# Optimization experiments

Hardware: AMD Instinct MI355X
Metric: run time of the kernel (lower is better)

The kernel has to match this reference:

```python
import jax, jax.numpy as jnp
import numpy as np

B, L, D = 8, 8192, 768  # trees, leaves per tree, d_in == d_hidden


def setup_inputs() -> dict:
    key = jax.random.key(0)
    ks = jax.random.split(key, 5)
    scale = 0.02  # keep gates out of saturation
    return {
        "leaf_emb": jax.random.normal(ks[0], (B, L, D), dtype=jnp.float32),
        "W_iou": jax.random.normal(ks[1], (3 * D, D), dtype=jnp.float32) * scale,
        "b_iou": jnp.zeros((3 * D,), dtype=jnp.float32),
        "U_iou": jax.random.normal(ks[2], (3 * D, D), dtype=jnp.float32) * scale,
        "W_f": jax.random.normal(ks[3], (D, D), dtype=jnp.float32) * scale,
        "b_f": jnp.zeros((D,), dtype=jnp.float32),
        "U_f": jax.random.normal(ks[4], (D, D), dtype=jnp.float32) * scale,
    }


def reference(leaf_emb, W_iou, b_iou, U_iou, W_f, b_f, U_f):
    """Child-Sum Tree-LSTM over a perfect binary tree, level-synchronous.

    Leaves: h = embedding, c = 0 (matches the torch module's leaf case).
    Internal node with children (l, r):
      h_sum = h_l + h_r; x = h_sum / 2
      i,o,u = split(W_iou x + b_iou + U_iou h_sum)
      f_k   = sigmoid(W_f x + b_f + U_f h_k)   per child
      c = sigmoid(i)*tanh(u) + f_l*c_l + f_r*c_r;  h = sigmoid(o)*tanh(c)
    Returns stacked (h_root, c_root): [2, B, D].
    """
    h = leaf_emb                      # [B, n, D]
    c = jnp.zeros_like(h)
    while h.shape[1] > 1:             # static trace-time loop over depth (13 levels)
        hl, hr = h[:, 0::2], h[:, 1::2]   # [B, n/2, D]
        cl, cr = c[:, 0::2], c[:, 1::2]
        h_sum = hl + hr
        x = h_sum * 0.5               # x_j = h_sum / num_children (==2)
        iou = jnp.einsum('bnd,gd->bng', x, W_iou) + b_iou \
            + jnp.einsum('bnd,gd->bng', h_sum, U_iou)
        i, o, u = jnp.split(iou, 3, axis=-1)
        wfx = jnp.einsum('bnd,hd->bnh', x, W_f) + b_f
        f_l = jax.nn.sigmoid(wfx + jnp.einsum('bnd,hd->bnh', hl, U_f))
        f_r = jax.nn.sigmoid(wfx + jnp.einsum('bnd,hd->bnh', hr, U_f))
        c = jax.nn.sigmoid(i) * jnp.tanh(u) + f_l * cl + f_r * cr
        h = jax.nn.sigmoid(o) * jnp.tanh(c)
    return jnp.stack([h[:, 0], c[:, 0]])  # [2, B, D]
```

## Files before the change

kernel.cpp:

```cpp
#include <hip/hip_runtime.h>


typedef _Float16 half8 __attribute__((ext_vector_type(8)));
typedef float f32x4 __attribute__((ext_vector_type(4)));

#define ROWB 1536
#define NT 24
#define BUFB 36864
#define MATB 1179648

__device__ __forceinline__ float sigm(float x){ return 1.f/(1.f+__expf(-x)); }
__device__ __forceinline__ float tanhfast(float x){ return 1.f - 2.f/(1.f+__expf(2.f*x)); }

__device__ __forceinline__ void gload16(const void* g, void* l){
  __builtin_amdgcn_global_load_lds((const __attribute__((address_space(1))) void*)g,
                                   (__attribute__((address_space(3))) void*)l, 16, 0, 0);
}

__global__ void prep_weights(const float* __restrict__ Wiou, const float* __restrict__ Uiou,
                             const float* __restrict__ Wf, const float* __restrict__ Uf,
                             _Float16* __restrict__ Bw)
{
    const int n1 = 2304 * 768, n2 = n1 + 589824, n3 = n2 + 589824;
    int stride = gridDim.x * blockDim.x;
    for (int idx = blockIdx.x * blockDim.x + threadIdx.x; idx < n3; idx += stride) {
        float v;
        if (idx < n1)      v = __fmaf_rn(0.5f, Wiou[idx], Uiou[idx]);
        else if (idx < n2) { int k = idx - n1; v = __fmaf_rn(0.5f, Wf[k], Uf[k]); }
        else               { int k = idx - n2; v = 0.5f * Wf[k]; }
        Bw[idx] = (_Float16)v;
    }
}

__global__ void cast_leaves(const float* __restrict__ x, _Float16* __restrict__ h, int n8)
{
    int stride = gridDim.x * blockDim.x;
    for (int i = blockIdx.x * blockDim.x + threadIdx.x; i < n8; i += stride) {
        float4 v0 = ((const float4*)x)[2 * i];
        float4 v1 = ((const float4*)x)[2 * i + 1];
        half8 o = { (_Float16)v0.x, (_Float16)v0.y, (_Float16)v0.z, (_Float16)v0.w,
                    (_Float16)v1.x, (_Float16)v1.y, (_Float16)v1.z, (_Float16)v1.w };
        ((half8*)h)[i] = o;
    }
}

__global__ __launch_bounds__(256, 2) void tree_level(
    const _Float16* __restrict__ Hc, const float* __restrict__ Cc,
    const _Float16* __restrict__ Bw,
    const float* __restrict__ biou, const float* __restrict__ bfv,
    _Float16* __restrict__ Hn, float* __restrict__ Cn,
    float* __restrict__ outH, float* __restrict__ outC,
    int M, int mblocks, int firstLevel, int finalLevel)
{
    __shared__ __align__(16) char smem[2 * BUFB];
    const int tid = threadIdx.x;
    const int lane = tid & 63;
    const int w = tid >> 6;
    const int wm = w >> 1;
    const int wd = w & 1;

    const int nwg = mblocks * 12;
    const int orig = blockIdx.x;
    const int xcd = orig & 7, qx = nwg >> 3, rx = nwg & 7;
    const int v = (xcd < rx ? xcd * (qx + 1) : rx * (qx + 1) + (xcd - rx) * qx) + (orig >> 3);
    const int d0c = v / mblocks;
    const int mb = v - d0c * mblocks;
    const int mBase = mb * 128;
    const int d0 = d0c * 64;

    const int l3 = lane >> 3, j = lane & 7;
    const int rbase = w * 8 + l3;
    const int jjA = j ^ l3;
    unsigned offH[4];
#pragma unroll
    for (int s = 0; s < 4; ++s) {
        int gr = mBase + s * 32 + rbase;
        if (gr >= M) gr = M - 1;
        offH[s] = (unsigned)(2 * gr + (jjA >> 2)) * ROWB + (jjA & 3) * 16;
    }
    const int pB = w * 8 + l3;
    const int jjB = j ^ (pB & 7);
    const unsigned offWcol = (unsigned)(d0 + 2 * pB + (jjB >> 2)) * ROWB + (jjB & 3) * 16;
    const int wK = w * 1024;

#define STAGE(bi, ko) do { \
    _Pragma("unroll") for (int s = 0; s < 4; ++s) \
        gload16((const char*)Hc + offH[s] + (ko), smem + (bi) * BUFB + s * 4096 + wK); \
    _Pragma("unroll") for (int s = 0; s < 5; ++s) \
        gload16((const char*)Bw + (size_t)s * MATB + offWcol + (ko), \
                smem + (bi) * BUFB + 16384 + s * 4096 + wK); \
} while (0)

    const int q = lane >> 4;
    const int lr = lane & 15;
    int offA[4], offB[2];
#pragma unroll
    for (int fm = 0; fm < 4; ++fm) {
        int r = wm * 64 + fm * 16 + lr;
        offA[fm] = r * 128 + ((q ^ (r & 7)) * 16);
    }
#pragma unroll
    for (int fd = 0; fd < 2; ++fd) {
        int cl = wd * 32 + fd * 16 + lr;
        int p = cl >> 1;
        int jb = ((cl & 1) * 4 + q) ^ (p & 7);
        offB[fd] = 16384 + p * 128 + jb * 16;
    }

    f32x4 acc[5][4][2];
#pragma unroll
    for (int g = 0; g < 5; ++g)
#pragma unroll
        for (int a = 0; a < 4; ++a)
#pragma unroll
            for (int b = 0; b < 2; ++b)
                acc[g][a][b] = (f32x4){0.f, 0.f, 0.f, 0.f};

    STAGE(0, 0);
    int cur = 0;
    for (int kt = 0; kt < NT; ++kt) {
        if (kt + 1 < NT) {
            STAGE(cur ^ 1, (kt + 1) * 64);
            asm volatile("s_waitcnt vmcnt(9)" ::: "memory");
        } else {
            asm volatile("s_waitcnt vmcnt(0)" ::: "memory");
        }
        __builtin_amdgcn_s_barrier();
        __builtin_amdgcn_sched_barrier(0);
        const char* bb = smem + cur * BUFB;
        half8 hl[4], hr[4];
#pragma unroll
        for (int fm = 0; fm < 4; ++fm) {
            hl[fm] = *(const half8*)(bb + offA[fm]);
            hr[fm] = *(const half8*)(bb + (offA[fm] ^ 64));
        }
        __builtin_amdgcn_s_setprio(1);
#pragma unroll
        for (int fd = 0; fd < 2; ++fd) {
            const char* bp = bb + offB[fd];
            half8 b0 = *(const half8*)(bp);
            half8 b1 = *(const half8*)(bp + 4096);
            half8 b2 = *(const half8*)(bp + 8192);
            half8 b3 = *(const half8*)(bp + 12288);
            half8 b4 = *(const half8*)(bp + 16384);
#pragma unroll
            for (int fm = 0; fm < 4; ++fm) {
                half8 hs = hl[fm] + hr[fm];
                acc[0][fm][fd] = __builtin_amdgcn_mfma_f32_16x16x32_f16(hs, b0, acc[0][fm][fd], 0, 0, 0);
                acc[1][fm][fd] = __builtin_amdgcn_mfma_f32_16x16x32_f16(hs, b1, acc[1][fm][fd], 0, 0, 0);
                acc[2][fm][fd] = __builtin_amdgcn_mfma_f32_16x16x32_f16(hs, b2, acc[2][fm][fd], 0, 0, 0);
                acc[3][fm][fd] = __builtin_amdgcn_mfma_f32_16x16x32_f16(hl[fm], b3, acc[3][fm][fd], 0, 0, 0);
                acc[3][fm][fd] = __builtin_amdgcn_mfma_f32_16x16x32_f16(hr[fm], b4, acc[3][fm][fd], 0, 0, 0);
                acc[4][fm][fd] = __builtin_amdgcn_mfma_f32_16x16x32_f16(hl[fm], b4, acc[4][fm][fd], 0, 0, 0);
                acc[4][fm][fd] = __builtin_amdgcn_mfma_f32_16x16x32_f16(hr[fm], b3, acc[4][fm][fd], 0, 0, 0);
            }
        }
        __builtin_amdgcn_s_setprio(0);
        if (kt + 1 < NT) __builtin_amdgcn_s_barrier();
        cur ^= 1;
    }

#pragma unroll
    for (int fd = 0; fd < 2; ++fd) {
        const int col = d0 + wd * 32 + fd * 16 + lr;
        const float bi = biou[col];
        const float bo = biou[768 + col];
        const float bu = biou[1536 + col];
        const float bf = bfv[col];
#pragma unroll
        for (int fm = 0; fm < 4; ++fm) {
            const int rb = mBase + wm * 64 + fm * 16 + q * 4;
#pragma unroll
            for (int r4 = 0; r4 < 4; ++r4) {
                int row = rb + r4;
                if (row < M) {
                    float iv = acc[0][fm][fd][r4] + bi;
                    float ov = acc[1][fm][fd][r4] + bo;
                    float uv = acc[2][fm][fd][r4] + bu;
                    float fl = sigm(acc[3][fm][fd][r4] + bf);
                    float fr = sigm(acc[4][fm][fd][r4] + bf);
                    float clv = 0.f, crv = 0.f;
                    if (!firstLevel) {
                        clv = Cc[(size_t)(2 * row) * 768 + col];
                        crv = Cc[(size_t)(2 * row + 1) * 768 + col];
                    }
                    float c = sigm(iv) * tanhfast(uv) + fl * clv + fr * crv;
                    float h = sigm(ov) * tanhfast(c);
                    if (finalLevel) {
                        outH[row * 768 + col] = h;
                        outC[row * 768 + col] = c;
                    } else {
                        Hn[(size_t)row * 768 + col] = (_Float16)h;
                        Cn[(size_t)row * 768 + col] = c;
                    }
                }
            }
        }
    }
}

extern "C" void kernel_launch(void* const* d_in, const int* in_sizes, int n_in,
                              void* d_out, int out_size, void* d_ws, size_t ws_size,
                              hipStream_t stream)
{
    const float* leaf = (const float*)d_in[0];
    const float* Wiou = (const float*)d_in[1];
    const float* biou = (const float*)d_in[2];
    const float* Uiou = (const float*)d_in[3];
    const float* Wf   = (const float*)d_in[4];
    const float* bfv  = (const float*)d_in[5];
    const float* Uf   = (const float*)d_in[6];

    char* ws = (char*)d_ws;
    _Float16* Bw = (_Float16*)(ws);
    _Float16* H0 = (_Float16*)(ws + 5898240);
    _Float16* H1 = (_Float16*)(ws + 106561536);
    float*    C0 = (float*)(ws + 156893184);
    float*    C1 = (float*)(ws + 257556480);

    prep_weights<<<1024, 256, 0, stream>>>(Wiou, Uiou, Wf, Uf, Bw);
    cast_leaves<<<2048, 256, 0, stream>>>(leaf, H0, 50331648 / 8);

    float* out = (float*)d_out;
    _Float16* Hc = H0; _Float16* Hn = H1;
    float* Cc = C1; float* Cn = C0;
    int rows = 65536, level = 0;
    while (rows > 8) {
        int M = rows >> 1;
        int fin = (M == 8) ? 1 : 0;
        int mblocks = (M + 127) / 128;
        tree_level<<<mblocks * 12, 256, 0, stream>>>(Hc, Cc, Bw, biou, bfv,
            Hn, Cn, fin ? out : (float*)nullptr, fin ? out + 6144 : (float*)nullptr,
            M, mblocks, level == 0 ? 1 : 0, fin);
        _Float16* th = Hc; Hc = Hn; Hn = th;
        float* tc = Cc; Cc = Cn; Cn = tc;
        rows = M; ++level;
    }
}
```

Measured before the change: 1.064 ms.

## Issue next-tile prefetch after LDS fragment reads and reorder block-to-tile mapping

The loop now reads all A and B fragments from LDS into registers, issues the global-to-LDS prefetch for the next K tile, and only then runs the MFMA chain. The wait becomes vmcnt(0) at the top of each iteration. The block index decomposition changes so that neighbouring workgroups share an M block across the 12 column chunks, which should improve reuse of the H rows in L2. The s_setprio hints are removed. This adds register pressure from holding 10 B fragments plus hs, and the full vmcnt(0) wait may expose load latency if the MFMA work does not cover it.

```diff
diff --git a/kernel.cpp b/kernel.cpp
--- a/kernel.cpp
+++ b/kernel.cpp
@@ -63,8 +63,8 @@
     const int orig = blockIdx.x;
     const int xcd = orig & 7, qx = nwg >> 3, rx = nwg & 7;
     const int v = (xcd < rx ? xcd * (qx + 1) : rx * (qx + 1) + (xcd - rx) * qx) + (orig >> 3);
-    const int d0c = v / mblocks;
-    const int mb = v - d0c * mblocks;
+    const int mb = v / 12;
+    const int d0c = v - mb * 12;
     const int mBase = mb * 128;
     const int d0 = d0c * 64;
 
@@ -119,43 +119,40 @@
     STAGE(0, 0);
     int cur = 0;
     for (int kt = 0; kt < NT; ++kt) {
-        if (kt + 1 < NT) {
-            STAGE(cur ^ 1, (kt + 1) * 64);
-            asm volatile("s_waitcnt vmcnt(9)" ::: "memory");
-        } else {
-            asm volatile("s_waitcnt vmcnt(0)" ::: "memory");
-        }
+        asm volatile("s_waitcnt vmcnt(0)" ::: "memory");
         __builtin_amdgcn_s_barrier();
-        __builtin_amdgcn_sched_barrier(0);
         const char* bb = smem + cur * BUFB;
-        half8 hl[4], hr[4];
+        half8 hl[4], hr[4], hs[4];
+        half8 bfrag[2][5];
 #pragma unroll
         for (int fm = 0; fm < 4; ++fm) {
             hl[fm] = *(const half8*)(bb + offA[fm]);
             hr[fm] = *(const half8*)(bb + (offA[fm] ^ 64));
         }
-        __builtin_amdgcn_s_setprio(1);
 #pragma unroll
         for (int fd = 0; fd < 2; ++fd) {
             const char* bp = bb + offB[fd];
-            half8 b0 = *(const half8*)(bp);
-            half8 b1 = *(const half8*)(bp + 4096);
-            half8 b2 = *(const half8*)(bp + 8192);
-            half8 b3 = *(const half8*)(bp + 12288);
-            half8 b4 = *(const half8*)(bp + 16384);
+#pragma unroll
+            for (int t = 0; t < 5; ++t)
+                bfrag[fd][t] = *(const half8*)(bp + t * 4096);
+        }
+        if (kt + 1 < NT) STAGE(cur ^ 1, (kt + 1) * 64);
+        __builtin_amdgcn_sched_barrier(0);
+#pragma unroll
+        for (int fm = 0; fm < 4; ++fm) hs[fm] = hl[fm] + hr[fm];
+#pragma unroll
+        for (int fd = 0; fd < 2; ++fd) {
 #pragma unroll
             for (int fm = 0; fm < 4; ++fm) {
-                half8 hs = hl[fm] + hr[fm];
-                acc[0][fm][fd] = __builtin_amdgcn_mfma_f32_16x16x32_f16(hs, b0, acc[0][fm][fd], 0, 0, 0);
-                acc[1][fm][fd] = __builtin_amdgcn_mfma_f32_16x16x32_f16(hs, b1, acc[1][fm][fd], 0, 0, 0);
-                acc[2][fm][fd] = __builtin_amdgcn_mfma_f32_16x16x32_f16(hs, b2, acc[2][fm][fd], 0, 0, 0);
-                acc[3][fm][fd] = __builtin_amdgcn_mfma_f32_16x16x32_f16(hl[fm], b3, acc[3][fm][fd], 0, 0, 0);
-                acc[3][fm][fd] = __builtin_amdgcn_mfma_f32_16x16x32_f16(hr[fm], b4, acc[3][fm][fd], 0, 0, 0);
-                acc[4][fm][fd] = __builtin_amdgcn_mfma_f32_16x16x32_f16(hl[fm], b4, acc[4][fm][fd], 0, 0, 0);
-                acc[4][fm][fd] = __builtin_amdgcn_mfma_f32_16x16x32_f16(hr[fm], b3, acc[4][fm][fd], 0, 0, 0);
+                acc[0][fm][fd] = __builtin_amdgcn_mfma_f32_16x16x32_f16(hs[fm], bfrag[fd][0], acc[0][fm][fd], 0, 0, 0);
+                acc[1][fm][fd] = __builtin_amdgcn_mfma_f32_16x16x32_f16(hs[fm], bfrag[fd][1], acc[1][fm][fd], 0, 0, 0);
+                acc[2][fm][fd] = __builtin_amdgcn_mfma_f32_16x16x32_f16(hs[fm], bfrag[fd][2], acc[2][fm][fd], 0, 0, 0);
+                acc[3][fm][fd] = __builtin_amdgcn_mfma_f32_16x16x32_f16(hl[fm], bfrag[fd][3], acc[3][fm][fd], 0, 0, 0);
+                acc[3][fm][fd] = __builtin_amdgcn_mfma_f32_16x16x32_f16(hr[fm], bfrag[fd][4], acc[3][fm][fd], 0, 0, 0);
+                acc[4][fm][fd] = __builtin_amdgcn_mfma_f32_16x16x32_f16(hl[fm], bfrag[fd][4], acc[4][fm][fd], 0, 0, 0);
+                acc[4][fm][fd] = __builtin_amdgcn_mfma_f32_16x16x32_f16(hr[fm], bfrag[fd][3], acc[4][fm][fd], 0, 0, 0);
             }
         }
-        __builtin_amdgcn_s_setprio(0);
         if (kt + 1 < NT) __builtin_amdgcn_s_barrier();
         cur ^= 1;
     }
```

After: 1.229 ms. 1.16x slower.

## Halve output-column tile to 32 and raise occupancy to three workgroups per CU

Applied to the files above, without the earlier changes.

Shrinks each workgroup's output tile from 64 to 32 hidden columns, doubling the grid and halving accumulator registers and weight shared-memory staging. This lets launch bounds target three resident workgroups per CU. It also changes the order of grid blocks, so that blocks sharing the same M rows land next to each other. It also re-maps the weight loads so fewer global-to-LDS copies are issued per stage, and loads hl/hr inside the MFMA loop. The cost is that each H tile is now read by twice as many workgroups and each A fragment is reused over fewer MFMAs.

```diff
diff --git a/kernel.cpp b/kernel.cpp
--- a/kernel.cpp
+++ b/kernel.cpp
@@ -6,8 +6,8 @@
 
 #define ROWB 1536
 #define NT 24
-#define BUFB 36864
-#define MATB 1179648
+#define BUFB 26624
+#define BOFF 16384
 
 __device__ __forceinline__ float sigm(float x){ return 1.f/(1.f+__expf(-x)); }
 __device__ __forceinline__ float tanhfast(float x){ return 1.f - 2.f/(1.f+__expf(2.f*x)); }
@@ -44,7 +44,7 @@
     }
 }
 
-__global__ __launch_bounds__(256, 2) void tree_level(
+__global__ __launch_bounds__(256, 3) void tree_level(
     const _Float16* __restrict__ Hc, const float* __restrict__ Cc,
     const _Float16* __restrict__ Bw,
     const float* __restrict__ biou, const float* __restrict__ bfv,
@@ -59,140 +59,134 @@
     const int wm = w >> 1;
     const int wd = w & 1;
 
-    const int nwg = mblocks * 12;
+    const int nwg = mblocks * 24;
     const int orig = blockIdx.x;
     const int xcd = orig & 7, qx = nwg >> 3, rx = nwg & 7;
     const int v = (xcd < rx ? xcd * (qx + 1) : rx * (qx + 1) + (xcd - rx) * qx) + (orig >> 3);
-    const int d0c = v / mblocks;
-    const int mb = v - d0c * mblocks;
+    const int mb = v / 24;
+    const int d0c = v - mb * 24;
     const int mBase = mb * 128;
-    const int d0 = d0c * 64;
+    const int d0 = d0c * 32;
 
     const int l3 = lane >> 3, j = lane & 7;
-    const int rbase = w * 8 + l3;
-    const int jjA = j ^ l3;
-    unsigned offH[4];
+    const int jj0 = j ^ l3;
+    unsigned offHa[4], offWb[3];
+    int dstA[4], dstB[3];
 #pragma unroll
     for (int s = 0; s < 4; ++s) {
-        int gr = mBase + s * 32 + rbase;
+        int u = s * 4 + w;
+        int gr = mBase + u * 8 + l3;
         if (gr >= M) gr = M - 1;
-        offH[s] = (unsigned)(2 * gr + (jjA >> 2)) * ROWB + (jjA & 3) * 16;
-    }
-    const int pB = w * 8 + l3;
-    const int jjB = j ^ (pB & 7);
-    const unsigned offWcol = (unsigned)(d0 + 2 * pB + (jjB >> 2)) * ROWB + (jjB & 3) * 16;
-    const int wK = w * 1024;
+        offHa[s] = (unsigned)(2 * gr + (jj0 >> 2)) * ROWB + (jj0 & 3) * 16;
+        dstA[s] = u * 1024;
+    }
+#pragma unroll
+    for (int s = 0; s < 3; ++s) {
+        int i = s * 4 + w;
+        if (i >= 10) i -= 2;
+        int t = i >> 1, half = i & 1;
+        int p = half * 8 + l3;
+        int cl = 2 * p + (jj0 >> 2);
+        offWb[s] = (unsigned)(t * 768 + d0 + cl) * ROWB + (jj0 & 3) * 16;
+        dstB[s] = BOFF + t * 2048 + half * 1024;
+    }
 
 #define STAGE(bi, ko) do { \
     _Pragma("unroll") for (int s = 0; s < 4; ++s) \
-        gload16((const char*)Hc + offH[s] + (ko), smem + (bi) * BUFB + s * 4096 + wK); \
-    _Pragma("unroll") for (int s = 0; s < 5; ++s) \
-        gload16((const char*)Bw + (size_t)s * MATB + offWcol + (ko), \
-                smem + (bi) * BUFB + 16384 + s * 4096 + wK); \
+        gload16((const char*)Hc + offHa[s] + (ko), smem + (bi) * BUFB + dstA[s]); \
+    _Pragma("unroll") for (int s = 0; s < 3; ++s) \
+        gload16((const char*)Bw + offWb[s] + (ko), smem + (bi) * BUFB + dstB[s]); \
 } while (0)
 
     const int q = lane >> 4;
     const int lr = lane & 15;
-    int offA[4], offB[2];
+    int offA[4];
 #pragma unroll
     for (int fm = 0; fm < 4; ++fm) {
         int r = wm * 64 + fm * 16 + lr;
         offA[fm] = r * 128 + ((q ^ (r & 7)) * 16);
     }
-#pragma unroll
-    for (int fd = 0; fd < 2; ++fd) {
-        int cl = wd * 32 + fd * 16 + lr;
+    int offB;
+    {
+        int cl = wd * 16 + lr;
         int p = cl >> 1;
         int jb = ((cl & 1) * 4 + q) ^ (p & 7);
-        offB[fd] = 16384 + p * 128 + jb * 16;
-    }
-
-    f32x4 acc[5][4][2];
+        offB = BOFF + p * 128 + jb * 16;
+    }
+
+    f32x4 acc[5][4];
 #pragma unroll
     for (int g = 0; g < 5; ++g)
 #pragma unroll
         for (int a = 0; a < 4; ++a)
-#pragma unroll
-            for (int b = 0; b < 2; ++b)
-                acc[g][a][b] = (f32x4){0.f, 0.f, 0.f, 0.f};
+            acc[g][a] = (f32x4){0.f, 0.f, 0.f, 0.f};
 
     STAGE(0, 0);
     int cur = 0;
     for (int kt = 0; kt < NT; ++kt) {
         if (kt + 1 < NT) {
             STAGE(cur ^ 1, (kt + 1) * 64);
-            asm volatile("s_waitcnt vmcnt(9)" ::: "memory");
+            asm volatile("s_waitcnt vmcnt(7)" ::: "memory");
         } else {
             asm volatile("s_waitcnt vmcnt(0)" ::: "memory");
         }
         __builtin_amdgcn_s_barrier();
         __builtin_amdgcn_sched_barrier(0);
         const char* bb = smem + cur * BUFB;
-        half8 hl[4], hr[4];
+        half8 b0 = *(const half8*)(bb + offB);
+        half8 b1 = *(const half8*)(bb + offB + 2048);
+        half8 b2 = *(const half8*)(bb + offB + 4096);
+        half8 b3 = *(const half8*)(bb + offB + 6144);
+        half8 b4 = *(const half8*)(bb + offB + 8192);
+        __builtin_amdgcn_s_setprio(1);
 #pragma unroll
         for (int fm = 0; fm < 4; ++fm) {
-            hl[fm] = *(const half8*)(bb + offA[fm]);
-            hr[fm] = *(const half8*)(bb + (offA[fm] ^ 64));
-        }
-        __builtin_amdgcn_s_setprio(1);
-#pragma unroll
-        for (int fd = 0; fd < 2; ++fd) {
-            const char* bp = bb + offB[fd];
-            half8 b0 = *(const half8*)(bp);
-            half8 b1 = *(const half8*)(bp + 4096);
-            half8 b2 = *(const half8*)(bp + 8192);
-            half8 b3 = *(const half8*)(bp + 12288);
-            half8 b4 = *(const half8*)(bp + 16384);
-#pragma unroll
-            for (int fm = 0; fm < 4; ++fm) {
-                half8 hs = hl[fm] + hr[fm];
-                acc[0][fm][fd] = __builtin_amdgcn_mfma_f32_16x16x32_f16(hs, b0, acc[0][fm][fd], 0, 0, 0);
-                acc[1][fm][fd] = __builtin_amdgcn_mfma_f32_16x16x32_f16(hs, b1, acc[1][fm][fd], 0, 0, 0);
-                acc[2][fm][fd] = __builtin_amdgcn_mfma_f32_16x16x32_f16(hs, b2, acc[2][fm][fd], 0, 0, 0);
-                acc[3][fm][fd] = __builtin_amdgcn_mfma_f32_16x16x32_f16(hl[fm], b3, acc[3][fm][fd], 0, 0, 0);
-                acc[3][fm][fd] = __builtin_amdgcn_mfma_f32_16x16x32_f16(hr[fm], b4, acc[3][fm][fd], 0, 0, 0);
-                acc[4][fm][fd] = __builtin_amdgcn_mfma_f32_16x16x32_f16(hl[fm], b4, acc[4][fm][fd], 0, 0, 0);
-                acc[4][fm][fd] = __builtin_amdgcn_mfma_f32_16x16x32_f16(hr[fm], b3, acc[4][fm][fd], 0, 0, 0);
-            }
+            half8 hl = *(const half8*)(bb + offA[fm]);
+            half8 hr = *(const half8*)(bb + (offA[fm] ^ 64));
+            acc[3][fm] = __builtin_amdgcn_mfma_f32_16x16x32_f16(hl, b3, acc[3][fm], 0, 0, 0);
+            acc[4][fm] = __builtin_amdgcn_mfma_f32_16x16x32_f16(hl, b4, acc[4][fm], 0, 0, 0);
+            half8 hs = hl + hr;
+            acc[0][fm] = __builtin_amdgcn_mfma_f32_16x16x32_f16(hs, b0, acc[0][fm], 0, 0, 0);
+            acc[1][fm] = __builtin_amdgcn_mfma_f32_16x16x32_f16(hs, b1, acc[1][fm], 0, 0, 0);
+            acc[2][fm] = __builtin_amdgcn_mfma_f32_16x16x32_f16(hs, b2, acc[2][fm], 0, 0, 0);
+            acc[3][fm] = __builtin_amdgcn_mfma_f32_16x16x32_f16(hr, b4, acc[3][fm], 0, 0, 0);
+            acc[4][fm] = __builtin_amdgcn_mfma_f32_16x16x32_f16(hr, b3, acc[4][fm], 0, 0, 0);
         }
         __builtin_amdgcn_s_setprio(0);
         if (kt + 1 < NT) __builtin_amdgcn_s_barrier();
         cur ^= 1;
     }
 
-#pragma unroll
-    for (int fd = 0; fd < 2; ++fd) {
-        const int col = d0 + wd * 32 + fd * 16 + lr;
-        const float bi = biou[col];
-        const float bo = biou[768 + col];
-        const float bu = biou[1536 + col];
-        const float bf = bfv[col];
-#pragma unroll
-        for (int fm = 0; fm < 4; ++fm) {
-            const int rb = mBase + wm * 64 + fm * 16 + q * 4;
-#pragma unroll
-            for (int r4 = 0; r4 < 4; ++r4) {
-                int row = rb + r4;
-                if (row < M) {
-                    float iv = acc[0][fm][fd][r4] + bi;
-                    float ov = acc[1][fm][fd][r4] + bo;
-                    float uv = acc[2][fm][fd][r4] + bu;
-                    float fl = sigm(acc[3][fm][fd][r4] + bf);
-                    float fr = sigm(acc[4][fm][fd][r4] + bf);
-                    float clv = 0.f, crv = 0.f;
-                    if (!firstLevel) {
-                        clv = Cc[(size_t)(2 * row) * 768 + col];
-                        crv = Cc[(size_t)(2 * row + 1) * 768 + col];
-                    }
-                    float c = sigm(iv) * tanhfast(uv) + fl * clv + fr * crv;
-                    float h = sigm(ov) * tanhfast(c);
-                    if (finalLevel) {
-                        outH[row * 768 + col] = h;
-                        outC[row * 768 + col] = c;
-                    } else {
-                        Hn[(size_t)row * 768 + col] = (_Float16)h;
-                        Cn[(size_t)row * 768 + col] = c;
-                    }
+    const int col = d0 + wd * 16 + lr;
+    const float bi = biou[col];
+    const float bo = biou[768 + col];
+    const float bu = biou[1536 + col];
+    const float bf = bfv[col];
+#pragma unroll
+    for (int fm = 0; fm < 4; ++fm) {
+        const int rb = mBase + wm * 64 + fm * 16 + q * 4;
+#pragma unroll
+        for (int r4 = 0; r4 < 4; ++r4) {
+            int row = rb + r4;
+            if (row < M) {
+                float iv = acc[0][fm][r4] + bi;
+                float ov = acc[1][fm][r4] + bo;
+                float uv = acc[2][fm][r4] + bu;
+                float fl = sigm(acc[3][fm][r4] + bf);
+                float fr = sigm(acc[4][fm][r4] + bf);
+                float clv = 0.f, crv = 0.f;
+                if (!firstLevel) {
+                    clv = Cc[(size_t)(2 * row) * 768 + col];
+                    crv = Cc[(size_t)(2 * row + 1) * 768 + col];
+                }
+                float c = sigm(iv) * tanhfast(uv) + fl * clv + fr * crv;
+                float h = sigm(ov) * tanhfast(c);
+                if (finalLevel) {
+                    outH[row * 768 + col] = h;
+                    outC[row * 768 + col] = c;
+                } else {
+                    Hn[(size_t)row * 768 + col] = (_Float16)h;
+                    Cn[(size_t)row * 768 + col] = c;
                 }
             }
         }
@@ -229,7 +223,7 @@
         int M = rows >> 1;
         int fin = (M == 8) ? 1 : 0;
         int mblocks = (M + 127) / 128;
-        tree_level<<<mblocks * 12, 256, 0, stream>>>(Hc, Cc, Bw, biou, bfv,
+        tree_level<<<mblocks * 24, 256, 0, stream>>>(Hc, Cc, Bw, biou, bfv,
             Hn, Cn, fin ? out : (float*)nullptr, fin ? out + 6144 : (float*)nullptr,
             M, mblocks, level == 0 ? 1 : 0, fin);
         _Float16* th = Hc; Hc = Hn; Hn = th;
```

Result: faster. 982.5 us (-7.6%).

## Factor forget-gate GEMMs via hs algebra and add narrow-tile kernel for small levels

Applied to the files above, without the earlier changes.

The forget gates are rewritten as W_f x + U_f h_l and W_f x + U_f(hs) - U_f h_l. Only U_f·h_l then needs a separate child operand, which cuts the per-k-step MFMA count from seven to six and drops the hr×b3/hr×b4 products. A new tree_small kernel with 32-column tiles and more blocks handles levels with M < 4096, to get more parallelism on the shallow levels. The large-level kernel also drops bounds checks and switches to an m-major block order. This adds one accumulator group of register pressure and some fp16 cancellation risk in the hs·U_f - h_l·U_f subtraction.

```diff
diff --git a/kernel.cpp b/kernel.cpp
--- a/kernel.cpp
+++ b/kernel.cpp
@@ -6,8 +6,8 @@
 
 #define ROWB 1536
 #define NT 24
-#define BUFB 36864
-#define MATB 1179648
+#define BUFA 36864
+#define BUFT 26624
 
 __device__ __forceinline__ float sigm(float x){ return 1.f/(1.f+__expf(-x)); }
 __device__ __forceinline__ float tanhfast(float x){ return 1.f - 2.f/(1.f+__expf(2.f*x)); }
@@ -26,8 +26,8 @@
     for (int idx = blockIdx.x * blockDim.x + threadIdx.x; idx < n3; idx += stride) {
         float v;
         if (idx < n1)      v = __fmaf_rn(0.5f, Wiou[idx], Uiou[idx]);
-        else if (idx < n2) { int k = idx - n1; v = __fmaf_rn(0.5f, Wf[k], Uf[k]); }
-        else               { int k = idx - n2; v = 0.5f * Wf[k]; }
+        else if (idx < n2) v = 0.5f * Wf[idx - n1];
+        else               v = Uf[idx - n2];
         Bw[idx] = (_Float16)v;
     }
 }
@@ -49,10 +49,9 @@
     const _Float16* __restrict__ Bw,
     const float* __restrict__ biou, const float* __restrict__ bfv,
     _Float16* __restrict__ Hn, float* __restrict__ Cn,
-    float* __restrict__ outH, float* __restrict__ outC,
-    int M, int mblocks, int firstLevel, int finalLevel)
-{
-    __shared__ __align__(16) char smem[2 * BUFB];
+    int M, int mblocks, int firstLevel)
+{
+    __shared__ __align__(16) char smem[2 * BUFA];
     const int tid = threadIdx.x;
     const int lane = tid & 63;
     const int w = tid >> 6;
@@ -63,71 +62,69 @@
     const int orig = blockIdx.x;
     const int xcd = orig & 7, qx = nwg >> 3, rx = nwg & 7;
     const int v = (xcd < rx ? xcd * (qx + 1) : rx * (qx + 1) + (xcd - rx) * qx) + (orig >> 3);
-    const int d0c = v / mblocks;
-    const int mb = v - d0c * mblocks;
+    const int mb = v / 12;
+    const int d0c = v - mb * 12;
     const int mBase = mb * 128;
     const int d0 = d0c * 64;
 
     const int l3 = lane >> 3, j = lane & 7;
+    const int jjA = j ^ l3;
     const int rbase = w * 8 + l3;
-    const int jjA = j ^ l3;
     unsigned offH[4];
 #pragma unroll
-    for (int s = 0; s < 4; ++s) {
-        int gr = mBase + s * 32 + rbase;
-        if (gr >= M) gr = M - 1;
-        offH[s] = (unsigned)(2 * gr + (jjA >> 2)) * ROWB + (jjA & 3) * 16;
-    }
+    for (int s = 0; s < 4; ++s)
+        offH[s] = (unsigned)(2 * (mBase + s * 32 + rbase) + (jjA >> 2)) * ROWB + (jjA & 3) * 16;
     const int pB = w * 8 + l3;
-    const int jjB = j ^ (pB & 7);
-    const unsigned offWcol = (unsigned)(d0 + 2 * pB + (jjB >> 2)) * ROWB + (jjB & 3) * 16;
+    unsigned offWb[5];
+#pragma unroll
+    for (int t = 0; t < 5; ++t)
+        offWb[t] = (unsigned)(t * 768 + d0 + 2 * pB + (jjA >> 2)) * ROWB + (jjA & 3) * 16;
     const int wK = w * 1024;
 
-#define STAGE(bi, ko) do { \
+#define STAGE_A(bi, ko) do { \
     _Pragma("unroll") for (int s = 0; s < 4; ++s) \
-        gload16((const char*)Hc + offH[s] + (ko), smem + (bi) * BUFB + s * 4096 + wK); \
-    _Pragma("unroll") for (int s = 0; s < 5; ++s) \
-        gload16((const char*)Bw + (size_t)s * MATB + offWcol + (ko), \
-                smem + (bi) * BUFB + 16384 + s * 4096 + wK); \
+        gload16((const char*)Hc + offH[s] + (ko), smem + (bi) * BUFA + s * 4096 + wK); \
+    _Pragma("unroll") for (int t = 0; t < 5; ++t) \
+        gload16((const char*)Bw + offWb[t] + (ko), smem + (bi) * BUFA + 16384 + t * 4096 + wK); \
 } while (0)
 
     const int q = lane >> 4;
-    const int lr = lane & 15;
+    const int lr16 = lane & 15;
     int offA[4], offB[2];
 #pragma unroll
     for (int fm = 0; fm < 4; ++fm) {
-        int r = wm * 64 + fm * 16 + lr;
+        int r = wm * 64 + fm * 16 + lr16;
         offA[fm] = r * 128 + ((q ^ (r & 7)) * 16);
     }
 #pragma unroll
     for (int fd = 0; fd < 2; ++fd) {
-        int cl = wd * 32 + fd * 16 + lr;
+        int cl = wd * 32 + fd * 16 + lr16;
         int p = cl >> 1;
         int jb = ((cl & 1) * 4 + q) ^ (p & 7);
         offB[fd] = 16384 + p * 128 + jb * 16;
     }
 
-    f32x4 acc[5][4][2];
-#pragma unroll
-    for (int g = 0; g < 5; ++g)
+    f32x4 acc[6][4][2];
+#pragma unroll
+    for (int g = 0; g < 6; ++g)
 #pragma unroll
         for (int a = 0; a < 4; ++a)
 #pragma unroll
-            for (int b = 0; b < 2; ++b)
-                acc[g][a][b] = (f32x4){0.f, 0.f, 0.f, 0.f};
-
-    STAGE(0, 0);
+            for (int b2 = 0; b2 < 2; ++b2)
+                acc[g][a][b2] = (f32x4){0.f, 0.f, 0.f, 0.f};
+
+    STAGE_A(0, 0);
     int cur = 0;
     for (int kt = 0; kt < NT; ++kt) {
         if (kt + 1 < NT) {
-            STAGE(cur ^ 1, (kt + 1) * 64);
+            STAGE_A(cur ^ 1, (kt + 1) * 64);
             asm volatile("s_waitcnt vmcnt(9)" ::: "memory");
         } else {
             asm volatile("s_waitcnt vmcnt(0)" ::: "memory");
         }
         __builtin_amdgcn_s_barrier();
         __builtin_amdgcn_sched_barrier(0);
-        const char* bb = smem + cur * BUFB;
+        const char* bb = smem + cur * BUFA;
         half8 hl[4], hr[4];
 #pragma unroll
         for (int fm = 0; fm < 4; ++fm) {
@@ -145,14 +142,13 @@
             half8 b4 = *(const half8*)(bp + 16384);
 #pragma unroll
             for (int fm = 0; fm < 4; ++fm) {
+                acc[4][fm][fd] = __builtin_amdgcn_mfma_f32_16x16x32_f16(hl[fm], b4, acc[4][fm][fd], 0, 0, 0);
                 half8 hs = hl[fm] + hr[fm];
                 acc[0][fm][fd] = __builtin_amdgcn_mfma_f32_16x16x32_f16(hs, b0, acc[0][fm][fd], 0, 0, 0);
                 acc[1][fm][fd] = __builtin_amdgcn_mfma_f32_16x16x32_f16(hs, b1, acc[1][fm][fd], 0, 0, 0);
                 acc[2][fm][fd] = __builtin_amdgcn_mfma_f32_16x16x32_f16(hs, b2, acc[2][fm][fd], 0, 0, 0);
-                acc[3][fm][fd] = __builtin_amdgcn_mfma_f32_16x16x32_f16(hl[fm], b3, acc[3][fm][fd], 0, 0, 0);
-                acc[3][fm][fd] = __builtin_amdgcn_mfma_f32_16x16x32_f16(hr[fm], b4, acc[3][fm][fd], 0, 0, 0);
-                acc[4][fm][fd] = __builtin_amdgcn_mfma_f32_16x16x32_f16(hl[fm], b4, acc[4][fm][fd], 0, 0, 0);
-                acc[4][fm][fd] = __builtin_amdgcn_mfma_f32_16x16x32_f16(hr[fm], b3, acc[4][fm][fd], 0, 0, 0);
+                acc[3][fm][fd] = __builtin_amdgcn_mfma_f32_16x16x32_f16(hs, b3, acc[3][fm][fd], 0, 0, 0);
+                acc[5][fm][fd] = __builtin_amdgcn_mfma_f32_16x16x32_f16(hs, b4, acc[5][fm][fd], 0, 0, 0);
             }
         }
         __builtin_amdgcn_s_setprio(0);
@@ -162,7 +158,7 @@
 
 #pragma unroll
     for (int fd = 0; fd < 2; ++fd) {
-        const int col = d0 + wd * 32 + fd * 16 + lr;
+        const int col = d0 + wd * 32 + fd * 16 + lr16;
         const float bi = biou[col];
         const float bo = biou[768 + col];
         const float bu = biou[1536 + col];
@@ -173,26 +169,166 @@
 #pragma unroll
             for (int r4 = 0; r4 < 4; ++r4) {
                 int row = rb + r4;
-                if (row < M) {
-                    float iv = acc[0][fm][fd][r4] + bi;
-                    float ov = acc[1][fm][fd][r4] + bo;
-                    float uv = acc[2][fm][fd][r4] + bu;
-                    float fl = sigm(acc[3][fm][fd][r4] + bf);
-                    float fr = sigm(acc[4][fm][fd][r4] + bf);
-                    float clv = 0.f, crv = 0.f;
-                    if (!firstLevel) {
-                        clv = Cc[(size_t)(2 * row) * 768 + col];
-                        crv = Cc[(size_t)(2 * row + 1) * 768 + col];
-                    }
-                    float c = sigm(iv) * tanhfast(uv) + fl * clv + fr * crv;
-                    float h = sigm(ov) * tanhfast(c);
-                    if (finalLevel) {
-                        outH[row * 768 + col] = h;
-                        outC[row * 768 + col] = c;
-                    } else {
-                        Hn[(size_t)row * 768 + col] = (_Float16)h;
-                        Cn[(size_t)row * 768 + col] = c;
-                    }
+                float iv = acc[0][fm][fd][r4] + bi;
+                float ov = acc[1][fm][fd][r4] + bo;
+                float uv = acc[2][fm][fd][r4] + bu;
+                float wfx = acc[3][fm][fd][r4] + bf;
+                float g6 = acc[4][fm][fd][r4];
+                float fl = sigm(wfx + g6);
+                float fr = sigm(wfx + acc[5][fm][fd][r4] - g6);
+                float clv = 0.f, crv = 0.f;
+                if (!firstLevel) {
+                    clv = Cc[(size_t)(2 * row) * 768 + col];
+                    crv = Cc[(size_t)(2 * row + 1) * 768 + col];
+                }
+                float c = sigm(iv) * tanhfast(uv) + fl * clv + fr * crv;
+                float h = sigm(ov) * tanhfast(c);
+                Hn[(size_t)row * 768 + col] = (_Float16)h;
+                Cn[(size_t)row * 768 + col] = c;
+            }
+        }
+    }
+}
+
+__global__ __launch_bounds__(256, 3) void tree_small(
+    const _Float16* __restrict__ Hc, const float* __restrict__ Cc,
+    const _Float16* __restrict__ Bw,
+    const float* __restrict__ biou, const float* __restrict__ bfv,
+    _Float16* __restrict__ Hn, float* __restrict__ Cn,
+    float* __restrict__ out,
+    int M, int finalLevel)
+{
+    __shared__ __align__(16) char smem[2 * BUFT];
+    const int tid = threadIdx.x;
+    const int lane = tid & 63;
+    const int w = tid >> 6;
+    const int wm = w >> 1;
+    const int wd = w & 1;
+    const int bid = blockIdx.x;
+    const int mb = bid / 24;
+    const int d0c = bid - mb * 24;
+    const int mBase = mb * 128;
+    const int d0 = d0c * 32;
+
+    const int l3 = lane >> 3, j = lane & 7;
+    const int jj0 = j ^ l3;
+
+    unsigned offWb[3];
+    int dstB[3];
+#pragma unroll
+    for (int s = 0; s < 3; ++s) {
+        int i = s * 4 + w;
+        if (i >= 10) i -= 2;
+        int t = i >> 1, half = i & 1;
+        int p = half * 8 + l3;
+        offWb[s] = (unsigned)(t * 768 + d0 + 2 * p + (jj0 >> 2)) * ROWB + (jj0 & 3) * 16;
+        dstB[s] = 16384 + t * 2048 + half * 1024;
+    }
+    unsigned offHa[4];
+    int dstA[4];
+#pragma unroll
+    for (int s = 0; s < 4; ++s) {
+        int u = s * 4 + w;
+        int gr = mBase + u * 8 + l3;
+        if (gr >= M) gr = M - 1;
+        offHa[s] = (unsigned)(2 * gr + (jj0 >> 2)) * ROWB + (jj0 & 3) * 16;
+        dstA[s] = u * 1024;
+    }
+
+#define STAGE_T(bi_, ko) do { \
+    _Pragma("unroll") for (int s = 0; s < 4; ++s) \
+        gload16((const char*)Hc + offHa[s] + (ko), smem + (bi_) * BUFT + dstA[s]); \
+    _Pragma("unroll") for (int s = 0; s < 3; ++s) \
+        gload16((const char*)Bw + offWb[s] + (ko), smem + (bi_) * BUFT + dstB[s]); \
+} while (0)
+
+    const int q = lane >> 4;
+    const int lr16 = lane & 15;
+    int offA[4];
+#pragma unroll
+    for (int fm = 0; fm < 4; ++fm) {
+        int r = wm * 64 + fm * 16 + lr16;
+        offA[fm] = r * 128 + ((q ^ (r & 7)) * 16);
+    }
+    int offB;
+    {
+        int cl = wd * 16 + lr16;
+        int p = cl >> 1;
+        int jb = ((cl & 1) * 4 + q) ^ (p & 7);
+        offB = 16384 + p * 128 + jb * 16;
+    }
+
+    f32x4 acc[6][4];
+#pragma unroll
+    for (int g = 0; g < 6; ++g)
+#pragma unroll
+        for (int a = 0; a < 4; ++a)
+            acc[g][a] = (f32x4){0.f, 0.f, 0.f, 0.f};
+
+    STAGE_T(0, 0);
+    int cur = 0;
+    for (int kt = 0; kt < NT; ++kt) {
+        if (kt + 1 < NT) {
+            STAGE_T(cur ^ 1, (kt + 1) * 64);
+            asm volatile("s_waitcnt vmcnt(7)" ::: "memory");
+        } else {
+            asm volatile("s_waitcnt vmcnt(0)" ::: "memory");
+        }
+        __builtin_amdgcn_s_barrier();
+        __builtin_amdgcn_sched_barrier(0);
+        const char* bb = smem + cur * BUFT;
+        half8 b0 = *(const half8*)(bb + offB);
+        half8 b1 = *(const half8*)(bb + offB + 2048);
+        half8 b2 = *(const half8*)(bb + offB + 4096);
+        half8 b3 = *(const half8*)(bb + offB + 6144);
+        half8 b4 = *(const half8*)(bb + offB + 8192);
+        __builtin_amdgcn_s_setprio(1);
+#pragma unroll
+        for (int fm = 0; fm < 4; ++fm) {
+            half8 hl = *(const half8*)(bb + offA[fm]);
+            half8 hr = *(const half8*)(bb + (offA[fm] ^ 64));
+            acc[4][fm] = __builtin_amdgcn_mfma_f32_16x16x32_f16(hl, b4, acc[4][fm], 0, 0, 0);
+            half8 hs = hl + hr;
+            acc[0][fm] = __builtin_amdgcn_mfma_f32_16x16x32_f16(hs, b0, acc[0][fm], 0, 0, 0);
+            acc[1][fm] = __builtin_amdgcn_mfma_f32_16x16x32_f16(hs, b1, acc[1][fm], 0, 0, 0);
+            acc[2][fm] = __builtin_amdgcn_mfma_f32_16x16x32_f16(hs, b2, acc[2][fm], 0, 0, 0);
+            acc[3][fm] = __builtin_amdgcn_mfma_f32_16x16x32_f16(hs, b3, acc[3][fm], 0, 0, 0);
+            acc[5][fm] = __builtin_amdgcn_mfma_f32_16x16x32_f16(hs, b4, acc[5][fm], 0, 0, 0);
+        }
+        __builtin_amdgcn_s_setprio(0);
+        if (kt + 1 < NT) __builtin_amdgcn_s_barrier();
+        cur ^= 1;
+    }
+
+    const int col = d0 + wd * 16 + lr16;
+    const float bi = biou[col];
+    const float bo = biou[768 + col];
+    const float bu = biou[1536 + col];
+    const float bf = bfv[col];
+#pragma unroll
+    for (int fm = 0; fm < 4; ++fm) {
+        const int rb = mBase + wm * 64 + fm * 16 + q * 4;
+#pragma unroll
+        for (int r4 = 0; r4 < 4; ++r4) {
+            int row = rb + r4;
+            if (row < M) {
+                float iv = acc[0][fm][r4] + bi;
+                float ov = acc[1][fm][r4] + bo;
+                float uv = acc[2][fm][r4] + bu;
+                float wfx = acc[3][fm][r4] + bf;
+                float g6 = acc[4][fm][r4];
+                float fl = sigm(wfx + g6);
+                float fr = sigm(wfx + acc[5][fm][r4] - g6);
+                float clv = Cc[(size_t)(2 * row) * 768 + col];
+                float crv = Cc[(size_t)(2 * row + 1) * 768 + col];
+                float c = sigm(iv) * tanhfast(uv) + fl * clv + fr * crv;
+                float h = sigm(ov) * tanhfast(c);
+                if (finalLevel) {
+                    out[row * 768 + col] = h;
+                    out[6144 + row * 768 + col] = c;
+                } else {
+                    Hn[(size_t)row * 768 + col] = (_Float16)h;
+                    Cn[(size_t)row * 768 + col] = c;
                 }
             }
         }
@@ -227,11 +363,16 @@
     int rows = 65536, level = 0;
     while (rows > 8) {
         int M = rows >> 1;
-        int fin = (M == 8) ? 1 : 0;
-        int mblocks = (M + 127) / 128;
-        tree_level<<<mblocks * 12, 256, 0, stream>>>(Hc, Cc, Bw, biou, bfv,
-            Hn, Cn, fin ? out : (float*)nullptr, fin ? out + 6144 : (float*)nullptr,
-            M, mblocks, level == 0 ? 1 : 0, fin);
+        if (M >= 4096) {
+            int mblocks = M / 128;
+            tree_level<<<mblocks * 12, 256, 0, stream>>>(Hc, Cc, Bw, biou, bfv,
+                Hn, Cn, M, mblocks, level == 0 ? 1 : 0);
+        } else {
+            int mblocks = (M + 127) / 128;
+            int fin = (M == 8) ? 1 : 0;
+            tree_small<<<mblocks * 24, 256, 0, stream>>>(Hc, Cc, Bw, biou, bfv,
+                Hn, Cn, out, M, fin);
+        }
         _Float16* th = Hc; Hc = Hn; Hn = th;
         float* tc = Cc; Cc = Cn; Cn = tc;
         rows = M; ++level;
```

New measurement: 1.074 ms. No clear change (+1.0%).
